# Kernel optimization log

Measured on AMD Instinct MI355X. Metric: run time of the kernel, lower is better.

Reference implementation:

```python
import jax, jax.numpy as jnp
import numpy as np

# The 16 differentiable binary logic gates used by difflogic are all of the form
# c0 + c1*a + c2*b + c3*(a*b). Rows are gate ids 0..15.
GATE_COEF = jnp.array([
    [0., 0., 0., 0.],    # 0: False
    [0., 0., 0., 1.],    # 1: a AND b
    [0., 1., 0., -1.],   # 2: a AND NOT b
    [0., 1., 0., 0.],    # 3: a
    [0., 0., 1., -1.],   # 4: NOT a AND b
    [0., 0., 1., 0.],    # 5: b
    [0., 1., 1., -2.],   # 6: XOR
    [0., 1., 1., -1.],   # 7: OR
    [1., -1., -1., 1.],  # 8: NOR
    [1., -1., -1., 2.],  # 9: XNOR
    [1., 0., -1., 0.],   # 10: NOT b
    [1., 0., -1., 1.],   # 11: a OR NOT b (b implies a)
    [1., -1., 0., 0.],   # 12: NOT a
    [1., -1., 0., 1.],   # 13: NOT a OR b (a implies b)
    [1., 0., 0., -1.],   # 14: NAND
    [1., 0., 0., 0.],    # 15: True
], dtype=jnp.float32)

BATCH = 256
IN_DIM = 1024
WIDTH = 64000
K = 10
TAU = 30.0


def _logic_layer(x, w, idx_a, idx_b):
    # x: [B, in_dim], w: [out, 16], idx_*: [out] int32
    a = x[:, idx_a]            # [B, out]
    b = x[:, idx_b]            # [B, out]
    coef = jax.nn.softmax(w, axis=-1) @ GATE_COEF   # [out, 4]
    return coef[:, 0] + coef[:, 1] * a + coef[:, 2] * b + coef[:, 3] * (a * b)


def setup_inputs() -> dict:
    key = jax.random.key(0)
    ks = jax.random.split(key, 10)
    x = jax.random.uniform(ks[0], (BATCH, IN_DIM), dtype=jnp.float32)
    w1 = jax.random.normal(ks[1], (WIDTH, 16), dtype=jnp.float32)
    w2 = jax.random.normal(ks[2], (WIDTH, 16), dtype=jnp.float32)
    w3 = jax.random.normal(ks[3], (WIDTH, 16), dtype=jnp.float32)
    idx_a1 = jax.random.randint(ks[4], (WIDTH,), 0, IN_DIM, dtype=jnp.int32)
    idx_b1 = jax.random.randint(ks[5], (WIDTH,), 0, IN_DIM, dtype=jnp.int32)
    idx_a2 = jax.random.randint(ks[6], (WIDTH,), 0, WIDTH, dtype=jnp.int32)
    idx_b2 = jax.random.randint(ks[7], (WIDTH,), 0, WIDTH, dtype=jnp.int32)
    idx_a3 = jax.random.randint(ks[8], (WIDTH,), 0, WIDTH, dtype=jnp.int32)
    idx_b3 = jax.random.randint(ks[9], (WIDTH,), 0, WIDTH, dtype=jnp.int32)
    return {"x": x, "w1": w1, "w2": w2, "w3": w3,
            "idx_a1": idx_a1, "idx_b1": idx_b1,
            "idx_a2": idx_a2, "idx_b2": idx_b2,
            "idx_a3": idx_a3, "idx_b3": idx_b3}


def reference(x, w1, w2, w3, idx_a1, idx_b1, idx_a2, idx_b2, idx_a3, idx_b3):
    h = _logic_layer(x, w1, idx_a1, idx_b1)
    h = _logic_layer(h, w2, idx_a2, idx_b2)
    h = _logic_layer(h, w3, idx_a3, idx_b3)
    # GroupSum: [B, WIDTH] -> [B, K, WIDTH//K] -> sum -> / tau
    return h.reshape(h.shape[0], K, -1).sum(axis=-1) / TAU
```

## Files before the change

kernel.cpp:

```cpp
#include <hip/hip_runtime.h>
#include <hip/hip_bf16.h>
#include <stdint.h>


#define BATCH   256
#define IN_DIM  1024
#define WIDTH   64000
#define NGROUP  10
#define GSIZE   6400
#define TAU     30.0f
#define NWAVE   16
#define GPW     8
#define GPB     (NWAVE*GPW)
#define NBLK    (WIDTH/GPB)

typedef unsigned short ushort_t;

static __device__ __forceinline__ float bf2f(ushort_t s) {
    return __uint_as_float((uint32_t)s << 16);
}
static __device__ __forceinline__ ushort_t f2bf(float f) {
    uint32_t u = __float_as_uint(f);
    return (ushort_t)((u + 0x7fffu + ((u >> 16) & 1u)) >> 16);
}

__global__ __launch_bounds__(256) void transpose_kernel(
    const float* __restrict__ x, ushort_t* __restrict__ xT)
{
    __shared__ float tile[64][65];
    const int c0 = (blockIdx.x & 15) * 64;
    const int b0 = (blockIdx.x >> 4) * 64;
    const int lt = threadIdx.x & 63;
    const int wt = threadIdx.x >> 6;
    for (int r = wt; r < 64; r += 4)
        tile[r][lt] = x[(b0 + r) * IN_DIM + c0 + lt];
    __syncthreads();
    for (int r = wt; r < 64; r += 4)
        xT[(c0 + r) * BATCH + b0 + lt] = f2bf(tile[lt][r]);
}

__global__ __launch_bounds__(256) void coef_kernel(
    const float* __restrict__ w1, const float* __restrict__ w2,
    const float* __restrict__ w3,
    float4* __restrict__ c1o, float4* __restrict__ c2o, float4* __restrict__ c3o)
{
    const int id = blockIdx.x * 256 + threadIdx.x;
    const int layer = id / WIDTH;
    const int j = id - layer * WIDTH;
    const float* w = (layer == 0) ? w1 : (layer == 1) ? w2 : w3;
    float4* cc     = (layer == 0) ? c1o : (layer == 1) ? c2o : c3o;

    const float4* w4 = (const float4*)(w + (size_t)j * 16);
    float4 q0 = w4[0], q1 = w4[1], q2 = w4[2], q3 = w4[3];
    float p[16] = {q0.x,q0.y,q0.z,q0.w, q1.x,q1.y,q1.z,q1.w,
                   q2.x,q2.y,q2.z,q2.w, q3.x,q3.y,q3.z,q3.w};
    float m = p[0];
    #pragma unroll
    for (int i = 1; i < 16; ++i) m = fmaxf(m, p[i]);
    float s = 0.f;
    #pragma unroll
    for (int i = 0; i < 16; ++i) { p[i] = __expf(p[i] - m); s += p[i]; }
    const float inv = 1.0f / s;

    float c0 = (p[8]+p[9]+p[10]+p[11]+p[12]+p[13]+p[14]+p[15]) * inv;
    float c1 = (p[2]+p[3]+p[6]+p[7] - p[8]-p[9]-p[12]-p[13]) * inv;
    float c2 = (p[4]+p[5]+p[6]+p[7] - p[8]-p[9]-p[10]-p[11]) * inv;
    float c3 = (p[1]-p[2]-p[4]-2.f*p[6]-p[7]+p[8]+2.f*p[9]+p[11]+p[13]-p[14]) * inv;
    cc[j] = make_float4(c0, c1, c2, c3);
}

template<bool FINAL>
__global__ __launch_bounds__(1024) void logic_layer_kernel(
    const ushort_t* __restrict__ in,
    const float4*   __restrict__ coefs,
    const int*      __restrict__ ia,
    const int*      __restrict__ ib,
    ushort_t*       __restrict__ out,
    float*          __restrict__ red_out)
{
    const int lane = threadIdx.x & 63;
    const int wave = __builtin_amdgcn_readfirstlane(threadIdx.x >> 6);
    const int jw = blockIdx.x * GPB + wave * GPW;

    int av[GPW], bv[GPW];
    #pragma unroll
    for (int u = 0; u < GPW; ++u) { av[u] = ia[jw + u]; bv[u] = ib[jw + u]; }

    float4 acc = make_float4(0.f, 0.f, 0.f, 0.f);

    #pragma unroll
    for (int u = 0; u < GPW; ++u) {
        const float4 c = coefs[jw + u];
        const ushort4 a4 = ((const ushort4*)(in + (size_t)av[u] * BATCH))[lane];
        const ushort4 b4 = ((const ushort4*)(in + (size_t)bv[u] * BATCH))[lane];
        const float Ax = bf2f(a4.x), Ay = bf2f(a4.y), Az = bf2f(a4.z), Aw = bf2f(a4.w);
        const float Bx = bf2f(b4.x), By = bf2f(b4.y), Bz = bf2f(b4.z), Bw = bf2f(b4.w);
        float4 r;
        r.x = fmaf(c.w, Ax * Bx, fmaf(c.z, Bx, fmaf(c.y, Ax, c.x)));
        r.y = fmaf(c.w, Ay * By, fmaf(c.z, By, fmaf(c.y, Ay, c.x)));
        r.z = fmaf(c.w, Az * Bz, fmaf(c.z, Bz, fmaf(c.y, Az, c.x)));
        r.w = fmaf(c.w, Aw * Bw, fmaf(c.z, Bw, fmaf(c.y, Aw, c.x)));
        if (FINAL) {
            acc.x += r.x; acc.y += r.y; acc.z += r.z; acc.w += r.w;
        } else {
            ushort4 o;
            o.x = f2bf(r.x); o.y = f2bf(r.y); o.z = f2bf(r.z); o.w = f2bf(r.w);
            ((ushort4*)(out + (size_t)(jw + u) * BATCH))[lane] = o;
        }
    }

    if (FINAL) {
        __shared__ float4 s[NWAVE][64];
        s[wave][lane] = acc;
        __syncthreads();
        if (wave == 0) {
            float4 t = s[0][lane];
            #pragma unroll
            for (int w = 1; w < NWAVE; ++w) {
                float4 q = s[w][lane];
                t.x += q.x; t.y += q.y; t.z += q.z; t.w += q.w;
            }
            const float sc = 1.0f / TAU;
            const int grp = (blockIdx.x * GPB) / GSIZE;
            const int b0 = lane * 4;
            atomicAdd(&red_out[(b0 + 0) * NGROUP + grp], t.x * sc);
            atomicAdd(&red_out[(b0 + 1) * NGROUP + grp], t.y * sc);
            atomicAdd(&red_out[(b0 + 2) * NGROUP + grp], t.z * sc);
            atomicAdd(&red_out[(b0 + 3) * NGROUP + grp], t.w * sc);
        }
    }
}

extern "C" void kernel_launch(void* const* d_in, const int* in_sizes, int n_in,
                              void* d_out, int out_size, void* d_ws, size_t ws_size,
                              hipStream_t stream)
{
    const float* x   = (const float*)d_in[0];
    const float* w1  = (const float*)d_in[1];
    const float* w2  = (const float*)d_in[2];
    const float* w3  = (const float*)d_in[3];
    const int*   ia1 = (const int*)d_in[4];
    const int*   ib1 = (const int*)d_in[5];
    const int*   ia2 = (const int*)d_in[6];
    const int*   ib2 = (const int*)d_in[7];
    const int*   ia3 = (const int*)d_in[8];
    const int*   ib3 = (const int*)d_in[9];
    float* out = (float*)d_out;

    char* ws = (char*)d_ws;
    ushort_t* xT = (ushort_t*)ws;
    ushort_t* h1 = (ushort_t*)(ws + ((size_t)IN_DIM * BATCH * 2));
    ushort_t* h2 = h1 + (size_t)WIDTH * BATCH;
    float*    c1 = (float*)(h2 + (size_t)WIDTH * BATCH);
    float*    c2 = c1 + (size_t)WIDTH * 4;
    float*    c3 = c2 + (size_t)WIDTH * 4;

    hipMemsetAsync(d_out, 0, (size_t)out_size * sizeof(float), stream);

    transpose_kernel<<<64, 256, 0, stream>>>(x, xT);
    coef_kernel<<<(3 * WIDTH) / 256, 256, 0, stream>>>(w1, w2, w3,
                                                       (float4*)c1, (float4*)c2, (float4*)c3);

    logic_layer_kernel<false><<<NBLK, 1024, 0, stream>>>(
        xT, (const float4*)c1, ia1, ib1, h1, nullptr);
    logic_layer_kernel<false><<<NBLK, 1024, 0, stream>>>(
        h1, (const float4*)c2, ia2, ib2, h2, nullptr);
    logic_layer_kernel<true><<<NBLK, 1024, 0, stream>>>(
        h2, (const float4*)c3, ia3, ib3, nullptr, out);
}
```

Measured before the change: 143.5 us.

## Fuse all stages into one persistent cooperative kernel with grid syncs

Replaces the memset, transpose, coefficient and three layer launches with a single cooperative kernel of 256 blocks x 1024 threads. Stages are separated by grid.sync, and the two hidden layers use a grid-stride loop over chunks of 8 gates. The goal is to remove the launch overhead and inter-kernel gaps of six stream operations. In exchange it adds grid-wide barrier cost, and a fixed 256-block grid that may give less latency hiding than the previous 500-block launches. The transpose is now done naively without a shared-memory tile.

```diff
diff --git a/kernel.cpp b/kernel.cpp
--- a/kernel.cpp
+++ b/kernel.cpp
@@ -1,6 +1,9 @@
 #include <hip/hip_runtime.h>
 #include <hip/hip_bf16.h>
+#include <hip/hip_cooperative_groups.h>
 #include <stdint.h>
+
+namespace cg = cooperative_groups;
 
 
 #define BATCH   256
@@ -9,10 +12,12 @@
 #define NGROUP  10
 #define GSIZE   6400
 #define TAU     30.0f
+#define NBLK    256
+#define NTHR    1024
 #define NWAVE   16
-#define GPW     8
-#define GPB     (NWAVE*GPW)
-#define NBLK    (WIDTH/GPB)
+#define NWAVES_G (NBLK*NWAVE)
+#define CHSZ    8
+#define NCHUNK  (WIDTH/CHSZ)
 
 typedef unsigned short ushort_t;
 
@@ -24,110 +29,133 @@
     return (ushort_t)((u + 0x7fffu + ((u >> 16) & 1u)) >> 16);
 }
 
-__global__ __launch_bounds__(256) void transpose_kernel(
-    const float* __restrict__ x, ushort_t* __restrict__ xT)
-{
-    __shared__ float tile[64][65];
-    const int c0 = (blockIdx.x & 15) * 64;
-    const int b0 = (blockIdx.x >> 4) * 64;
-    const int lt = threadIdx.x & 63;
-    const int wt = threadIdx.x >> 6;
-    for (int r = wt; r < 64; r += 4)
-        tile[r][lt] = x[(b0 + r) * IN_DIM + c0 + lt];
-    __syncthreads();
-    for (int r = wt; r < 64; r += 4)
-        xT[(c0 + r) * BATCH + b0 + lt] = f2bf(tile[lt][r]);
+static __device__ __forceinline__ float4 gate4(float4 c, ushort4 a4, ushort4 b4) {
+    const float Ax = bf2f(a4.x), Ay = bf2f(a4.y), Az = bf2f(a4.z), Aw = bf2f(a4.w);
+    const float Bx = bf2f(b4.x), By = bf2f(b4.y), Bz = bf2f(b4.z), Bw = bf2f(b4.w);
+    float4 r;
+    r.x = fmaf(c.w, Ax * Bx, fmaf(c.z, Bx, fmaf(c.y, Ax, c.x)));
+    r.y = fmaf(c.w, Ay * By, fmaf(c.z, By, fmaf(c.y, Ay, c.x)));
+    r.z = fmaf(c.w, Az * Bz, fmaf(c.z, Bz, fmaf(c.y, Az, c.x)));
+    r.w = fmaf(c.w, Aw * Bw, fmaf(c.z, Bw, fmaf(c.y, Aw, c.x)));
+    return r;
 }
 
-__global__ __launch_bounds__(256) void coef_kernel(
+static __device__ __forceinline__ void layer_pass(
+    const ushort_t* __restrict__ in, const float4* __restrict__ coefs,
+    const int* __restrict__ ia, const int* __restrict__ ib,
+    ushort_t* __restrict__ outp, int lane, int gwave)
+{
+    for (int ch = gwave; ch < NCHUNK; ch += NWAVES_G) {
+        const int jw = ch * CHSZ;
+        int av[CHSZ], bv[CHSZ];
+        #pragma unroll
+        for (int u = 0; u < CHSZ; ++u) { av[u] = ia[jw + u]; bv[u] = ib[jw + u]; }
+        #pragma unroll
+        for (int u = 0; u < CHSZ; ++u) {
+            const float4 c = coefs[jw + u];
+            const ushort4 a4 = ((const ushort4*)(in + (size_t)av[u] * BATCH))[lane];
+            const ushort4 b4 = ((const ushort4*)(in + (size_t)bv[u] * BATCH))[lane];
+            const float4 r = gate4(c, a4, b4);
+            ushort4 o;
+            o.x = f2bf(r.x); o.y = f2bf(r.y); o.z = f2bf(r.z); o.w = f2bf(r.w);
+            ((ushort4*)(outp + (size_t)(jw + u) * BATCH))[lane] = o;
+        }
+    }
+}
+
+__global__ __launch_bounds__(NTHR, 4) void fused_kernel(
+    const float* __restrict__ x,
     const float* __restrict__ w1, const float* __restrict__ w2,
     const float* __restrict__ w3,
-    float4* __restrict__ c1o, float4* __restrict__ c2o, float4* __restrict__ c3o)
+    const int* __restrict__ ia1, const int* __restrict__ ib1,
+    const int* __restrict__ ia2, const int* __restrict__ ib2,
+    const int* __restrict__ ia3, const int* __restrict__ ib3,
+    ushort_t* __restrict__ xT, ushort_t* __restrict__ h1,
+    ushort_t* __restrict__ h2,
+    float4* __restrict__ c1, float4* __restrict__ c2, float4* __restrict__ c3,
+    float* __restrict__ out)
 {
-    const int id = blockIdx.x * 256 + threadIdx.x;
-    const int layer = id / WIDTH;
-    const int j = id - layer * WIDTH;
-    const float* w = (layer == 0) ? w1 : (layer == 1) ? w2 : w3;
-    float4* cc     = (layer == 0) ? c1o : (layer == 1) ? c2o : c3o;
+    cg::grid_group grid = cg::this_grid();
+    const int lane = threadIdx.x & 63;
+    const int wave = __builtin_amdgcn_readfirstlane((int)(threadIdx.x >> 6));
+    const int blk  = blockIdx.x;
+    const int tid  = blk * NTHR + threadIdx.x;
+    const int gwave = blk * NWAVE + wave;
 
-    const float4* w4 = (const float4*)(w + (size_t)j * 16);
-    float4 q0 = w4[0], q1 = w4[1], q2 = w4[2], q3 = w4[3];
-    float p[16] = {q0.x,q0.y,q0.z,q0.w, q1.x,q1.y,q1.z,q1.w,
-                   q2.x,q2.y,q2.z,q2.w, q3.x,q3.y,q3.z,q3.w};
-    float m = p[0];
-    #pragma unroll
-    for (int i = 1; i < 16; ++i) m = fmaxf(m, p[i]);
-    float s = 0.f;
-    #pragma unroll
-    for (int i = 0; i < 16; ++i) { p[i] = __expf(p[i] - m); s += p[i]; }
-    const float inv = 1.0f / s;
+    if (tid < 3 * WIDTH) {
+        const int layer = tid / WIDTH;
+        const int j = tid - layer * WIDTH;
+        const float* w = (layer == 0) ? w1 : (layer == 1) ? w2 : w3;
+        float4* cc     = (layer == 0) ? c1 : (layer == 1) ? c2 : c3;
+        const float4* w4 = (const float4*)(w + (size_t)j * 16);
+        float4 q0 = w4[0], q1 = w4[1], q2 = w4[2], q3 = w4[3];
+        float p[16] = {q0.x,q0.y,q0.z,q0.w, q1.x,q1.y,q1.z,q1.w,
+                       q2.x,q2.y,q2.z,q2.w, q3.x,q3.y,q3.z,q3.w};
+        float m = p[0];
+        #pragma unroll
+        for (int i = 1; i < 16; ++i) m = fmaxf(m, p[i]);
+        float s = 0.f;
+        #pragma unroll
+        for (int i = 0; i < 16; ++i) { p[i] = __expf(p[i] - m); s += p[i]; }
+        const float inv = 1.0f / s;
+        float g0 = (p[8]+p[9]+p[10]+p[11]+p[12]+p[13]+p[14]+p[15]) * inv;
+        float g1 = (p[2]+p[3]+p[6]+p[7] - p[8]-p[9]-p[12]-p[13]) * inv;
+        float g2 = (p[4]+p[5]+p[6]+p[7] - p[8]-p[9]-p[10]-p[11]) * inv;
+        float g3 = (p[1]-p[2]-p[4]-2.f*p[6]-p[7]+p[8]+2.f*p[9]+p[11]+p[13]-p[14]) * inv;
+        cc[j] = make_float4(g0, g1, g2, g3);
+    }
 
-    float c0 = (p[8]+p[9]+p[10]+p[11]+p[12]+p[13]+p[14]+p[15]) * inv;
-    float c1 = (p[2]+p[3]+p[6]+p[7] - p[8]-p[9]-p[12]-p[13]) * inv;
-    float c2 = (p[4]+p[5]+p[6]+p[7] - p[8]-p[9]-p[10]-p[11]) * inv;
-    float c3 = (p[1]-p[2]-p[4]-2.f*p[6]-p[7]+p[8]+2.f*p[9]+p[11]+p[13]-p[14]) * inv;
-    cc[j] = make_float4(c0, c1, c2, c3);
-}
+    {
+        const int c = tid >> 8;
+        const int b = tid & 255;
+        xT[tid] = f2bf(x[b * IN_DIM + c]);
+    }
 
-template<bool FINAL>
-__global__ __launch_bounds__(1024) void logic_layer_kernel(
-    const ushort_t* __restrict__ in,
-    const float4*   __restrict__ coefs,
-    const int*      __restrict__ ia,
-    const int*      __restrict__ ib,
-    ushort_t*       __restrict__ out,
-    float*          __restrict__ red_out)
-{
-    const int lane = threadIdx.x & 63;
-    const int wave = __builtin_amdgcn_readfirstlane(threadIdx.x >> 6);
-    const int jw = blockIdx.x * GPB + wave * GPW;
+    if (tid < BATCH * NGROUP) out[tid] = 0.f;
 
-    int av[GPW], bv[GPW];
-    #pragma unroll
-    for (int u = 0; u < GPW; ++u) { av[u] = ia[jw + u]; bv[u] = ib[jw + u]; }
+    grid.sync();
 
+    layer_pass(xT, c1, ia1, ib1, h1, lane, gwave);
+    grid.sync();
+
+    layer_pass(h1, c2, ia2, ib2, h2, lane, gwave);
+    grid.sync();
+
+    __shared__ float4 s[NWAVE][64];
     float4 acc = make_float4(0.f, 0.f, 0.f, 0.f);
-
-    #pragma unroll
-    for (int u = 0; u < GPW; ++u) {
-        const float4 c = coefs[jw + u];
-        const ushort4 a4 = ((const ushort4*)(in + (size_t)av[u] * BATCH))[lane];
-        const ushort4 b4 = ((const ushort4*)(in + (size_t)bv[u] * BATCH))[lane];
-        const float Ax = bf2f(a4.x), Ay = bf2f(a4.y), Az = bf2f(a4.z), Aw = bf2f(a4.w);
-        const float Bx = bf2f(b4.x), By = bf2f(b4.y), Bz = bf2f(b4.z), Bw = bf2f(b4.w);
-        float4 r;
-        r.x = fmaf(c.w, Ax * Bx, fmaf(c.z, Bx, fmaf(c.y, Ax, c.x)));
-        r.y = fmaf(c.w, Ay * By, fmaf(c.z, By, fmaf(c.y, Ay, c.x)));
-        r.z = fmaf(c.w, Az * Bz, fmaf(c.z, Bz, fmaf(c.y, Az, c.x)));
-        r.w = fmaf(c.w, Aw * Bw, fmaf(c.z, Bw, fmaf(c.y, Aw, c.x)));
-        if (FINAL) {
-            acc.x += r.x; acc.y += r.y; acc.z += r.z; acc.w += r.w;
-        } else {
-            ushort4 o;
-            o.x = f2bf(r.x); o.y = f2bf(r.y); o.z = f2bf(r.z); o.w = f2bf(r.w);
-            ((ushort4*)(out + (size_t)(jw + u) * BATCH))[lane] = o;
+    if (blk < 250) {
+        #pragma unroll
+        for (int k = 0; k < 2; ++k) {
+            const int jw = (blk * 32 + wave * 2 + k) * CHSZ;
+            int av[CHSZ], bv[CHSZ];
+            #pragma unroll
+            for (int u = 0; u < CHSZ; ++u) { av[u] = ia3[jw + u]; bv[u] = ib3[jw + u]; }
+            #pragma unroll
+            for (int u = 0; u < CHSZ; ++u) {
+                const float4 c = c3[jw + u];
+                const ushort4 a4 = ((const ushort4*)(h2 + (size_t)av[u] * BATCH))[lane];
+                const ushort4 b4 = ((const ushort4*)(h2 + (size_t)bv[u] * BATCH))[lane];
+                const float4 r = gate4(c, a4, b4);
+                acc.x += r.x; acc.y += r.y; acc.z += r.z; acc.w += r.w;
+            }
         }
     }
-
-    if (FINAL) {
-        __shared__ float4 s[NWAVE][64];
-        s[wave][lane] = acc;
-        __syncthreads();
-        if (wave == 0) {
-            float4 t = s[0][lane];
-            #pragma unroll
-            for (int w = 1; w < NWAVE; ++w) {
-                float4 q = s[w][lane];
-                t.x += q.x; t.y += q.y; t.z += q.z; t.w += q.w;
-            }
-            const float sc = 1.0f / TAU;
-            const int grp = (blockIdx.x * GPB) / GSIZE;
-            const int b0 = lane * 4;
-            atomicAdd(&red_out[(b0 + 0) * NGROUP + grp], t.x * sc);
-            atomicAdd(&red_out[(b0 + 1) * NGROUP + grp], t.y * sc);
-            atomicAdd(&red_out[(b0 + 2) * NGROUP + grp], t.z * sc);
-            atomicAdd(&red_out[(b0 + 3) * NGROUP + grp], t.w * sc);
+    s[wave][lane] = acc;
+    __syncthreads();
+    if (wave == 0 && blk < 250) {
+        float4 t = s[0][lane];
+        #pragma unroll
+        for (int w = 1; w < NWAVE; ++w) {
+            float4 q = s[w][lane];
+            t.x += q.x; t.y += q.y; t.z += q.z; t.w += q.w;
         }
+        const float sc = 1.0f / TAU;
+        const int grp = (blk * 256) / GSIZE;
+        const int b0 = lane * 4;
+        atomicAdd(&out[(b0 + 0) * NGROUP + grp], t.x * sc);
+        atomicAdd(&out[(b0 + 1) * NGROUP + grp], t.y * sc);
+        atomicAdd(&out[(b0 + 2) * NGROUP + grp], t.z * sc);
+        atomicAdd(&out[(b0 + 3) * NGROUP + grp], t.w * sc);
     }
 }
 
@@ -155,16 +183,14 @@
     float*    c2 = c1 + (size_t)WIDTH * 4;
     float*    c3 = c2 + (size_t)WIDTH * 4;
 
-    hipMemsetAsync(d_out, 0, (size_t)out_size * sizeof(float), stream);
-
-    transpose_kernel<<<64, 256, 0, stream>>>(x, xT);
-    coef_kernel<<<(3 * WIDTH) / 256, 256, 0, stream>>>(w1, w2, w3,
-                                                       (float4*)c1, (float4*)c2, (float4*)c3);
-
-    logic_layer_kernel<false><<<NBLK, 1024, 0, stream>>>(
-        xT, (const float4*)c1, ia1, ib1, h1, nullptr);
-    logic_layer_kernel<false><<<NBLK, 1024, 0, stream>>>(
-        h1, (const float4*)c2, ia2, ib2, h2, nullptr);
-    logic_layer_kernel<true><<<NBLK, 1024, 0, stream>>>(
-        h2, (const float4*)c3, ia3, ib3, nullptr, out);
+    void* args[] = {
+        (void*)&x, (void*)&w1, (void*)&w2, (void*)&w3,
+        (void*)&ia1, (void*)&ib1, (void*)&ia2, (void*)&ib2,
+        (void*)&ia3, (void*)&ib3,
+        (void*)&xT, (void*)&h1, (void*)&h2,
+        (void*)&c1, (void*)&c2, (void*)&c3,
+        (void*)&out
+    };
+    hipLaunchCooperativeKernel((void*)fused_kernel, dim3(NBLK), dim3(NTHR),
+                               args, 0, stream);
 }
```

Result: slower. 260.0 us (+81.1%).
